# Kernel optimization log

Measured on AMD Instinct MI355X. Metric: run time of the kernel, lower is better.

The kernel has to match this reference:

```python
import jax, jax.numpy as jnp
import numpy as np

B, T, C, H = 4, 4096, 1024, 64

def setup_inputs() -> dict:
    key = jax.random.key(0)
    k1, k2, k3, k4, k5 = jax.random.split(key, 5)
    scale = 0.02
    return {
        "x": jax.random.normal(k1, (B, T, C), dtype=jnp.float32),
        "head_bias": jax.random.normal(k2, (T, T), dtype=jnp.float32) * 0.1,
        "w_k": jax.random.normal(k3, (C, H), dtype=jnp.float32) * scale,
        "w_q": jax.random.normal(k4, (C, H), dtype=jnp.float32) * scale,
        "w_v": jax.random.normal(k5, (C, H), dtype=jnp.float32) * scale,
    }

def reference(x, head_bias, w_k, w_q, w_v):
    # x: (B,T,C) ; projections: (B,T,H)
    k = jnp.einsum('btc,ch->bth', x, w_k)
    q = jnp.einsum('btc,ch->bth', x, w_q)
    v = jnp.einsum('btc,ch->bth', x, w_v)
    Tq = x.shape[1]
    # scores: (B,T,T) with RPE bias and causal mask
    scores = jnp.einsum('bqh,bkh->bqk', q, k) * (k.shape[-1] ** -0.5)
    scores = scores + head_bias[None, :, :]
    causal = jnp.tril(jnp.ones((Tq, Tq), dtype=bool))
    scores = jnp.where(causal[None, :, :], scores, -jnp.inf)
    weights = jax.nn.softmax(scores, axis=-1)
    out = jnp.einsum('bqk,bkh->bqh', weights, v)
    return out
```

## Files before the change

### kernel.cpp

```cpp
#include <hip/hip_runtime.h>
#include <hip/hip_bf16.h>


#define T_DIM 4096
#define C_DIM 1024
#define CK    256

typedef __attribute__((ext_vector_type(8))) short s16x8;
typedef __attribute__((ext_vector_type(4))) float f32x4;
typedef __attribute__((ext_vector_type(2))) unsigned int u32x2;

__device__ __forceinline__ short f2bf(float f) {
    unsigned u = __builtin_bit_cast(unsigned, f);
    u += 0x7FFFu + ((u >> 16) & 1u);
    return (short)(u >> 16);
}
__device__ __forceinline__ unsigned pack2(float a, float b) {
    unsigned ua = __builtin_bit_cast(unsigned, a);
    unsigned ub = __builtin_bit_cast(unsigned, b);
    ua += 0x7FFFu + ((ua >> 16) & 1u);
    ub += 0x7FFFu + ((ub >> 16) & 1u);
    return __builtin_amdgcn_perm(ub, ua, 0x07060302u);
}
__device__ __forceinline__ float bf2f(short s) {
    unsigned u = ((unsigned)(unsigned short)s) << 16;
    return __builtin_bit_cast(float, u);
}
__device__ __forceinline__ int chunk_off(int qt) {
    int g = qt >> 4, r = qt & 15;
    return qt + 8 * g * (g - 1) + r * g;
}

__global__ __launch_bounds__(256) void prep_frag(
    const float* __restrict__ wk, const float* __restrict__ wq,
    const float* __restrict__ wv, short* __restrict__ wfrag)
{
    int ksAll = blockIdx.x, mat = blockIdx.y;
    const float* w = (mat == 0) ? wk : ((mat == 1) ? wq : wv);
    float sc = (mat == 1) ? 0.125f : 1.0f;
    int nt = threadIdx.x >> 6, lane = threadIdx.x & 63;
    int quad = lane >> 4, l15 = lane & 15;
    int h = nt * 16 + l15;
    int cb = ksAll * 32 + quad * 8;
    s16x8 v;
    #pragma unroll
    for (int j = 0; j < 8; ++j) v[j] = f2bf(w[(cb + j) * 64 + h] * sc);
    *(s16x8*)&wfrag[((ksAll * 12 + mat * 4 + nt) * 64 + lane) * 8] = v;
}

__global__ __launch_bounds__(512, 2) void proj_fused(
    const float* __restrict__ x, const short* __restrict__ wfrag,
    short* __restrict__ qb, short* __restrict__ kfrag, short* __restrict__ vfrag)
{
    __shared__ __align__(16) short comb[4][16][136];
    __shared__ __align__(16) short vsep[64][72];

    int tid = threadIdx.x;
    int w = tid >> 6, lane = tid & 63;
    int g = w & 3, h = w >> 2;
    int l15 = lane & 15, quad = lane >> 4;
    int m0 = blockIdx.x * 64;
    int row0 = m0 + g * 16;

    f32x4 acc[12];
    #pragma unroll
    for (int i = 0; i < 12; ++i) acc[i] = (f32x4){0.f, 0.f, 0.f, 0.f};

    const float* xrow = x + (size_t)(row0 + l15) * C_DIM + h * 512;

    #pragma unroll 1
    for (int ks = 0; ks < 16; ++ks) {
        int ksAll = h * 16 + ks;
        const s16x8* fb = (const s16x8*)&wfrag[(size_t)(ksAll * 12 * 64 + lane) * 8];
        f32x4 x0 = *(const f32x4*)(xrow + ks * 32 + quad * 8);
        f32x4 x1 = *(const f32x4*)(xrow + ks * 32 + quad * 8 + 4);
        s16x8 af;
        unsigned p0 = pack2(x0[0], x0[1]), p1 = pack2(x0[2], x0[3]);
        unsigned p2 = pack2(x1[0], x1[1]), p3 = pack2(x1[2], x1[3]);
        af[0] = (short)p0; af[1] = (short)(p0 >> 16);
        af[2] = (short)p1; af[3] = (short)(p1 >> 16);
        af[4] = (short)p2; af[5] = (short)(p2 >> 16);
        af[6] = (short)p3; af[7] = (short)(p3 >> 16);
        #pragma unroll
        for (int f = 0; f < 12; ++f) {
            s16x8 bf = fb[f * 64];
            acc[f] = __builtin_amdgcn_mfma_f32_16x16x32_bf16(af, bf, acc[f], 0, 0, 0);
        }
    }

    if (h == 1) {
        #pragma unroll
        for (int f = 0; f < 8; ++f)
            #pragma unroll
            for (int r = 0; r < 4; ++r)
                comb[g][quad * 4 + r][(f >> 2) * 64 + (f & 3) * 16 + l15] = f2bf(acc[f][r]);
        #pragma unroll
        for (int f = 8; f < 12; ++f)
            #pragma unroll
            for (int r = 0; r < 4; ++r)
                vsep[(f & 3) * 16 + l15][g * 16 + quad * 4 + r] = f2bf(acc[f][r]);
    }
    __syncthreads();
    if (h == 0) {
        #pragma unroll
        for (int f = 0; f < 8; ++f)
            #pragma unroll
            for (int r = 0; r < 4; ++r) {
                int col = (f >> 2) * 64 + (f & 3) * 16 + l15, rr = quad * 4 + r;
                comb[g][rr][col] = f2bf(acc[f][r] + bf2f(comb[g][rr][col]));
            }
        #pragma unroll
        for (int f = 8; f < 12; ++f)
            #pragma unroll
            for (int r = 0; r < 4; ++r) {
                int hh = (f & 3) * 16 + l15, kk = g * 16 + quad * 4 + r;
                vsep[hh][kk] = f2bf(acc[f][r] + bf2f(vsep[hh][kk]));
            }
    }
    __syncthreads();

    int b = m0 >> 12, t0 = m0 & 4095;
    {
        int row = tid >> 3, ch = tid & 7;
        s16x8 v = *(const s16x8*)&comb[row >> 4][row & 15][64 + ch * 8];
        *(s16x8*)&qb[(size_t)(m0 + row) * 64 + ch * 8] = v;
    }
    {
        int kt = w & 3, ks = w >> 2;
        s16x8 v = *(const s16x8*)&comb[kt][l15][ks * 32 + quad * 8];
        *(s16x8*)&kfrag[(size_t)(((b * 256 + (t0 >> 4) + kt) * 2 + ks) * 64 + lane) * 8] = v;
    }
    {
        int kt32 = w & 1, nt = w >> 1;
        s16x8 v = *(const s16x8*)&vsep[nt * 16 + l15][kt32 * 32 + quad * 8];
        *(s16x8*)&vfrag[(size_t)(((b * 128 + (t0 >> 5) + kt32) * 4 + nt) * 64 + lane) * 8] = v;
    }
}

#define LOADST(AK, VB, k0) do {                                               \
    int _kt16 = (k0) >> 4;                                                    \
    _Pragma("unroll")                                                         \
    for (int _n = 0; _n < 2; ++_n) {                                          \
        const short* _kp = kfb + (size_t)((_kt16 + _n) * 2) * 512 + lane * 8; \
        AK[_n * 2]     = *(const s16x8*)_kp;                                  \
        AK[_n * 2 + 1] = *(const s16x8*)(_kp + 512);                          \
    }                                                                         \
    _Pragma("unroll")                                                         \
    for (int _n = 0; _n < 2; ++_n)                                            \
        VB[_n] = *(const f32x4*)&brow[(k0) + _n * 16 + quad * 4];             \
} while (0)

#define COMPUTEST(AK, VB, k0) do {                                            \
    int _kt32 = (k0) >> 5;                                                    \
    s16x8 _bv[4];                                                             \
    _Pragma("unroll")                                                         \
    for (int _n = 0; _n < 4; ++_n)                                            \
        _bv[_n] = *(const s16x8*)(vfb + (size_t)(_kt32 * 4 + _n) * 512 + lane * 8); \
    f32x4 _aS[2];                                                             \
    _Pragma("unroll")                                                         \
    for (int _n = 0; _n < 2; ++_n) {                                          \
        _aS[_n] = (f32x4){0.f, 0.f, 0.f, 0.f};                                \
        _aS[_n] = __builtin_amdgcn_mfma_f32_16x16x32_bf16(AK[_n*2],   aq0, _aS[_n], 0, 0, 0); \
        _aS[_n] = __builtin_amdgcn_mfma_f32_16x16x32_bf16(AK[_n*2+1], aq1, _aS[_n], 0, 0, 0); \
    }                                                                         \
    _Pragma("unroll")                                                         \
    for (int _n = 0; _n < 2; ++_n) {                                          \
        float _sv[4];                                                         \
        _Pragma("unroll")                                                     \
        for (int _r = 0; _r < 4; ++_r) {                                      \
            _sv[_r] = _aS[_n][_r] + VB[_n][_r];                               \
            if (mask_on && ((k0) + _n * 16 + quad * 4 + _r > strip0 + l15))   \
                _sv[_r] = -__builtin_inff();                                  \
            float _p = __expf(_sv[_r]);                                       \
            _sv[_r] = _p;                                                     \
            l_sum += _p;                                                      \
        }                                                                     \
        u32x2 _d;                                                             \
        _d[0] = pack2(_sv[0], _sv[1]);                                        \
        _d[1] = pack2(_sv[2], _sv[3]);                                        \
        *(u32x2*)&plds[w][l15][_n * 16 + quad * 4] = _d;                      \
    }                                                                         \
    s16x8 _ap = *(const s16x8*)&plds[w][l15][quad * 8];                       \
    _Pragma("unroll")                                                         \
    for (int _n = 0; _n < 4; ++_n)                                            \
        accO[_n] = __builtin_amdgcn_mfma_f32_16x16x32_bf16(_ap, _bv[_n], accO[_n], 0, 0, 0); \
} while (0)

__global__ __launch_bounds__(256, 4) void flash_part(
    const short* __restrict__ qb, const short* __restrict__ kfrag,
    const short* __restrict__ vfrag, const float* __restrict__ bias,
    short* __restrict__ po)
{
    int qt = blockIdx.x, c = blockIdx.y;
    if (c > (qt >> 4)) return;
    int q0 = qt * 16;
    int kstart = c * CK;
    int kend = min(kstart + CK, q0 + 16);

    __shared__ __align__(16) short plds[4][16][40];

    int w = threadIdx.x >> 6, lane = threadIdx.x & 63;
    int b = w;
    int l15 = lane & 15, quad = lane >> 4;
    int strip0 = q0;

    const short* qrow = qb + (size_t)(b * T_DIM + strip0 + l15) * 64;
    s16x8 aq0 = *(const s16x8*)(qrow + quad * 8);
    s16x8 aq1 = *(const s16x8*)(qrow + 32 + quad * 8);

    float l_sum = 0.f;
    f32x4 accO[4];
    #pragma unroll
    for (int nt = 0; nt < 4; ++nt) accO[nt] = (f32x4){0.f, 0.f, 0.f, 0.f};

    const float* brow = bias + (size_t)(strip0 + l15) * T_DIM;
    const short* kfb = kfrag + (size_t)b * 256 * 2 * 512;
    const short* vfb = vfrag + (size_t)b * 128 * 4 * 512;
    bool mask_on = (kend > strip0);

    s16x8 akA[4], akB[4];
    f32x4 vbA[2], vbB[2];
    int k0 = kstart;
    LOADST(akA, vbA, k0);
    while (true) {
        int k1 = k0 + 32;
        bool more = (k1 < kend);
        if (more) LOADST(akB, vbB, k1);
        COMPUTEST(akA, vbA, k0);
        if (!more) break;
        k0 = k1; k1 = k0 + 32;
        bool more2 = (k1 < kend);
        if (more2) LOADST(akA, vbA, k1);
        COMPUTEST(akB, vbB, k0);
        if (!more2) break;
        k0 = k1;
    }

    l_sum += __shfl_xor(l_sum, 16, 64);
    l_sum += __shfl_xor(l_sum, 32, 64);

    short* base = po + (size_t)((chunk_off(qt) + c) * 4 + b) * 1040;
    #pragma unroll
    for (int nt = 0; nt < 4; ++nt)
        #pragma unroll
        for (int r = 0; r < 4; ++r)
            base[(quad * 4 + r) * 64 + nt * 16 + l15] = f2bf(accO[nt][r]);
    if (quad == 0) base[1024 + l15] = f2bf(l_sum);
}

__global__ __launch_bounds__(256) void flash_reduce(
    const short* __restrict__ po, float* __restrict__ out)
{
    int idx = blockIdx.x * 256 + threadIdx.x;
    int row = idx >> 4, c4 = idx & 15;
    int b = row >> 12, t = row & 4095;
    int qt = t >> 4, rloc = t & 15;
    int nc = (t >> 8) + 1;
    int off = chunk_off(qt);
    float o0 = 0.f, o1 = 0.f, o2 = 0.f, o3 = 0.f, l = 0.f;
    #pragma unroll 1
    for (int cc = 0; cc < nc; ++cc) {
        const short* base = po + (size_t)((off + cc) * 4 + b) * 1040;
        const short* p = &base[rloc * 64 + c4 * 4];
        o0 += bf2f(p[0]); o1 += bf2f(p[1]); o2 += bf2f(p[2]); o3 += bf2f(p[3]);
        l += bf2f(base[1024 + rloc]);
    }
    float inv = 1.0f / l;
    f32x4 res = (f32x4){o0 * inv, o1 * inv, o2 * inv, o3 * inv};
    *(f32x4*)&out[(size_t)row * 64 + c4 * 4] = res;
}

extern "C" void kernel_launch(void* const* d_in, const int* in_sizes, int n_in,
                              void* d_out, int out_size, void* d_ws, size_t ws_size,
                              hipStream_t stream) {
    (void)in_sizes; (void)n_in; (void)out_size; (void)ws_size;
    const float* x    = (const float*)d_in[0];
    const float* bias = (const float*)d_in[1];
    const float* wk   = (const float*)d_in[2];
    const float* wq   = (const float*)d_in[3];
    const float* wv   = (const float*)d_in[4];
    float* out = (float*)d_out;

    short* wfrag = (short*)d_ws;
    short* qb    = wfrag + 196608;
    short* kfrag = qb + 1048576;
    short* vfrag = kfrag + 1048576;
    short* po    = vfrag + 1048576;

    prep_frag<<<dim3(32, 3), dim3(256), 0, stream>>>(wk, wq, wv, wfrag);
    proj_fused<<<dim3(256), dim3(512), 0, stream>>>(x, wfrag, qb, kfrag, vfrag);
    flash_part<<<dim3(256, 16), dim3(256), 0, stream>>>(qb, kfrag, vfrag, bias, po);
    flash_reduce<<<dim3(1024), dim3(256), 0, stream>>>(po, out);
}
```

Baseline: 222.7 us.

## Stage x tile and bias strip through LDS in projection and flash kernels

The projection kernel now processes 32 rows per block with 256 threads and first loads the x tile with fully coalesced float4 reads, converts it to bf16 and stores it in shared memory, so MFMA A-fragments come from LDS instead of strided global loads. The flash partial kernel cooperatively copies its 16x256 bias strip into LDS once per block with coalesced reads rather than having each wave read the bias row inside the loop. This removes uncoalesced global traffic and repeated bias reads across the four batch waves. In exchange it adds LDS usage (about 66KB union in proj, about 17KB in flash), which may limit occupancy, plus extra barriers.

Result: faster. 202.5 us (-9.1%).

```diff
diff --git a/kernel.cpp b/kernel.cpp
--- a/kernel.cpp
+++ b/kernel.cpp
@@ -48,57 +48,64 @@
     *(s16x8*)&wfrag[((ksAll * 12 + mat * 4 + nt) * 64 + lane) * 8] = v;
 }
 
-__global__ __launch_bounds__(512, 2) void proj_fused(
+union ProjSmem {
+    short xs[32][1032];
+    struct {
+        short comb[2][16][136];
+        short vsep[64][40];
+    } c;
+};
+
+__global__ __launch_bounds__(256, 2) void proj_fused(
     const float* __restrict__ x, const short* __restrict__ wfrag,
     short* __restrict__ qb, short* __restrict__ kfrag, short* __restrict__ vfrag)
 {
-    __shared__ __align__(16) short comb[4][16][136];
-    __shared__ __align__(16) short vsep[64][72];
+    __shared__ __align__(16) ProjSmem sm;
 
     int tid = threadIdx.x;
     int w = tid >> 6, lane = tid & 63;
-    int g = w & 3, h = w >> 2;
+    int rt = w >> 1, h = w & 1;
     int l15 = lane & 15, quad = lane >> 4;
-    int m0 = blockIdx.x * 64;
-    int row0 = m0 + g * 16;
+    int m0 = blockIdx.x * 32;
+
+    #pragma unroll 8
+    for (int p = 0; p < 32; ++p) {
+        f32x4 v = *(const f32x4*)&x[(size_t)(m0 + p) * C_DIM + tid * 4];
+        u32x2 d;
+        d[0] = pack2(v[0], v[1]);
+        d[1] = pack2(v[2], v[3]);
+        *(u32x2*)&sm.xs[p][tid * 4] = d;
+    }
+    __syncthreads();
 
     f32x4 acc[12];
     #pragma unroll
     for (int i = 0; i < 12; ++i) acc[i] = (f32x4){0.f, 0.f, 0.f, 0.f};
-
-    const float* xrow = x + (size_t)(row0 + l15) * C_DIM + h * 512;
 
     #pragma unroll 1
     for (int ks = 0; ks < 16; ++ks) {
         int ksAll = h * 16 + ks;
+        s16x8 af = *(const s16x8*)&sm.xs[rt * 16 + l15][ksAll * 32 + quad * 8];
         const s16x8* fb = (const s16x8*)&wfrag[(size_t)(ksAll * 12 * 64 + lane) * 8];
-        f32x4 x0 = *(const f32x4*)(xrow + ks * 32 + quad * 8);
-        f32x4 x1 = *(const f32x4*)(xrow + ks * 32 + quad * 8 + 4);
-        s16x8 af;
-        unsigned p0 = pack2(x0[0], x0[1]), p1 = pack2(x0[2], x0[3]);
-        unsigned p2 = pack2(x1[0], x1[1]), p3 = pack2(x1[2], x1[3]);
-        af[0] = (short)p0; af[1] = (short)(p0 >> 16);
-        af[2] = (short)p1; af[3] = (short)(p1 >> 16);
-        af[4] = (short)p2; af[5] = (short)(p2 >> 16);
-        af[6] = (short)p3; af[7] = (short)(p3 >> 16);
         #pragma unroll
         for (int f = 0; f < 12; ++f) {
             s16x8 bf = fb[f * 64];
             acc[f] = __builtin_amdgcn_mfma_f32_16x16x32_bf16(af, bf, acc[f], 0, 0, 0);
         }
     }
+    __syncthreads();
 
     if (h == 1) {
         #pragma unroll
         for (int f = 0; f < 8; ++f)
             #pragma unroll
             for (int r = 0; r < 4; ++r)
-                comb[g][quad * 4 + r][(f >> 2) * 64 + (f & 3) * 16 + l15] = f2bf(acc[f][r]);
+                sm.c.comb[rt][quad * 4 + r][(f >> 2) * 64 + (f & 3) * 16 + l15] = f2bf(acc[f][r]);
         #pragma unroll
         for (int f = 8; f < 12; ++f)
             #pragma unroll
             for (int r = 0; r < 4; ++r)
-                vsep[(f & 3) * 16 + l15][g * 16 + quad * 4 + r] = f2bf(acc[f][r]);
+                sm.c.vsep[(f & 3) * 16 + l15][rt * 16 + quad * 4 + r] = f2bf(acc[f][r]);
     }
     __syncthreads();
     if (h == 0) {
@@ -107,37 +114,38 @@
             #pragma unroll
             for (int r = 0; r < 4; ++r) {
                 int col = (f >> 2) * 64 + (f & 3) * 16 + l15, rr = quad * 4 + r;
-                comb[g][rr][col] = f2bf(acc[f][r] + bf2f(comb[g][rr][col]));
+                sm.c.comb[rt][rr][col] = f2bf(acc[f][r] + bf2f(sm.c.comb[rt][rr][col]));
             }
         #pragma unroll
         for (int f = 8; f < 12; ++f)
             #pragma unroll
             for (int r = 0; r < 4; ++r) {
-                int hh = (f & 3) * 16 + l15, kk = g * 16 + quad * 4 + r;
-                vsep[hh][kk] = f2bf(acc[f][r] + bf2f(vsep[hh][kk]));
+                int hh = (f & 3) * 16 + l15, kk = rt * 16 + quad * 4 + r;
+                sm.c.vsep[hh][kk] = f2bf(acc[f][r] + bf2f(sm.c.vsep[hh][kk]));
             }
     }
     __syncthreads();
 
     int b = m0 >> 12, t0 = m0 & 4095;
+    int t016 = t0 >> 4, kt32 = t0 >> 5;
     {
         int row = tid >> 3, ch = tid & 7;
-        s16x8 v = *(const s16x8*)&comb[row >> 4][row & 15][64 + ch * 8];
+        s16x8 v = *(const s16x8*)&sm.c.comb[row >> 4][row & 15][64 + ch * 8];
         *(s16x8*)&qb[(size_t)(m0 + row) * 64 + ch * 8] = v;
     }
     {
-        int kt = w & 3, ks = w >> 2;
-        s16x8 v = *(const s16x8*)&comb[kt][l15][ks * 32 + quad * 8];
-        *(s16x8*)&kfrag[(size_t)(((b * 256 + (t0 >> 4) + kt) * 2 + ks) * 64 + lane) * 8] = v;
+        int kt = w & 1, ks = w >> 1;
+        s16x8 v = *(const s16x8*)&sm.c.comb[kt][l15][ks * 32 + quad * 8];
+        *(s16x8*)&kfrag[(size_t)(((b * 256 + t016 + kt) * 2 + ks) * 64 + lane) * 8] = v;
     }
     {
-        int kt32 = w & 1, nt = w >> 1;
-        s16x8 v = *(const s16x8*)&vsep[nt * 16 + l15][kt32 * 32 + quad * 8];
-        *(s16x8*)&vfrag[(size_t)(((b * 128 + (t0 >> 5) + kt32) * 4 + nt) * 64 + lane) * 8] = v;
-    }
-}
-
-#define LOADST(AK, VB, k0) do {                                               \
+        int nt = w;
+        s16x8 v = *(const s16x8*)&sm.c.vsep[nt * 16 + l15][quad * 8];
+        *(s16x8*)&vfrag[(size_t)(((b * 128 + kt32) * 4 + nt) * 64 + lane) * 8] = v;
+    }
+}
+
+#define LOADK(AK, k0) do {                                                    \
     int _kt16 = (k0) >> 4;                                                    \
     _Pragma("unroll")                                                         \
     for (int _n = 0; _n < 2; ++_n) {                                          \
@@ -145,13 +153,11 @@
         AK[_n * 2]     = *(const s16x8*)_kp;                                  \
         AK[_n * 2 + 1] = *(const s16x8*)(_kp + 512);                          \
     }                                                                         \
-    _Pragma("unroll")                                                         \
-    for (int _n = 0; _n < 2; ++_n)                                            \
-        VB[_n] = *(const f32x4*)&brow[(k0) + _n * 16 + quad * 4];             \
 } while (0)
 
-#define COMPUTEST(AK, VB, k0) do {                                            \
+#define COMPUTEK(AK, k0) do {                                                 \
     int _kt32 = (k0) >> 5;                                                    \
+    int _kl = (k0) - kstart;                                                  \
     s16x8 _bv[4];                                                             \
     _Pragma("unroll")                                                         \
     for (int _n = 0; _n < 4; ++_n)                                            \
@@ -165,10 +171,11 @@
     }                                                                         \
     _Pragma("unroll")                                                         \
     for (int _n = 0; _n < 2; ++_n) {                                          \
+        f32x4 _vb = *(const f32x4*)&blds[l15][_kl + _n * 16 + quad * 4];      \
         float _sv[4];                                                         \
         _Pragma("unroll")                                                     \
         for (int _r = 0; _r < 4; ++_r) {                                      \
-            _sv[_r] = _aS[_n][_r] + VB[_n][_r];                               \
+            _sv[_r] = _aS[_n][_r] + _vb[_r];                                  \
             if (mask_on && ((k0) + _n * 16 + quad * 4 + _r > strip0 + l15))   \
                 _sv[_r] = -__builtin_inff();                                  \
             float _p = __expf(_sv[_r]);                                       \
@@ -197,6 +204,7 @@
     int kstart = c * CK;
     int kend = min(kstart + CK, q0 + 16);
 
+    __shared__ __align__(16) float blds[16][260];
     __shared__ __align__(16) short plds[4][16][40];
 
     int w = threadIdx.x >> 6, lane = threadIdx.x & 63;
@@ -204,6 +212,11 @@
     int l15 = lane & 15, quad = lane >> 4;
     int strip0 = q0;
 
+    #pragma unroll
+    for (int p = 0; p < 4; ++p)
+        *(f32x4*)&blds[p * 4 + w][lane * 4] =
+            *(const f32x4*)&bias[(size_t)(q0 + p * 4 + w) * T_DIM + kstart + lane * 4];
+
     const short* qrow = qb + (size_t)(b * T_DIM + strip0 + l15) * 64;
     s16x8 aq0 = *(const s16x8*)(qrow + quad * 8);
     s16x8 aq1 = *(const s16x8*)(qrow + 32 + quad * 8);
@@ -213,25 +226,25 @@
     #pragma unroll
     for (int nt = 0; nt < 4; ++nt) accO[nt] = (f32x4){0.f, 0.f, 0.f, 0.f};
 
-    const float* brow = bias + (size_t)(strip0 + l15) * T_DIM;
     const short* kfb = kfrag + (size_t)b * 256 * 2 * 512;
     const short* vfb = vfrag + (size_t)b * 128 * 4 * 512;
     bool mask_on = (kend > strip0);
 
+    __syncthreads();
+
     s16x8 akA[4], akB[4];
-    f32x4 vbA[2], vbB[2];
     int k0 = kstart;
-    LOADST(akA, vbA, k0);
+    LOADK(akA, k0);
     while (true) {
         int k1 = k0 + 32;
         bool more = (k1 < kend);
-        if (more) LOADST(akB, vbB, k1);
-        COMPUTEST(akA, vbA, k0);
+        if (more) LOADK(akB, k1);
+        COMPUTEK(akA, k0);
         if (!more) break;
         k0 = k1; k1 = k0 + 32;
         bool more2 = (k1 < kend);
-        if (more2) LOADST(akA, vbA, k1);
-        COMPUTEST(akB, vbB, k0);
+        if (more2) LOADK(akA, k1);
+        COMPUTEK(akB, k0);
         if (!more2) break;
         k0 = k1;
     }
@@ -288,7 +301,7 @@
     short* po    = vfrag + 1048576;
 
     prep_frag<<<dim3(32, 3), dim3(256), 0, stream>>>(wk, wq, wv, wfrag);
-    proj_fused<<<dim3(256), dim3(512), 0, stream>>>(x, wfrag, qb, kfrag, vfrag);
+    proj_fused<<<dim3(512), dim3(256), 0, stream>>>(x, wfrag, qb, kfrag, vfrag);
     flash_part<<<dim3(256, 16), dim3(256), 0, stream>>>(qb, kfrag, vfrag, bias, po);
     flash_reduce<<<dim3(1024), dim3(256), 0, stream>>>(po, out);
 }
```
